# Kernel tuning notes

Measured on AMD Instinct MI355X. Metric: run time of the kernel, lower is better.

The kernel has to match this reference:

```python
import jax, jax.numpy as jnp
import numpy as np


def setup_inputs() -> dict:
    key = jax.random.key(0)
    k1, k2 = jax.random.split(key)
    b, d = 8192, 256
    x = jax.random.normal(k1, (b, d), dtype=jnp.float32)
    dc = jax.random.uniform(k2, (b, d), dtype=jnp.float32)
    dc_param = jnp.array([0.05], dtype=jnp.float32)
    return {"x": x, "dc": dc, "dc_param": dc_param}


def reference(x, dc, dc_param):
    # Faithful to torch: sim[i,j] = 1 / mean_k[(1-p)*(x[i,k]-x[j,k])^2
    #                                        + p*exp(1-dc[i,k])*exp(1-dc[j,k])]
    # Expanded to GEMMs to avoid the O(b^2*d) broadcast intermediate:
    #   mean_k (x_i - x_j)^2 = (|x_i|^2 + |x_j|^2 - 2 x_i.x_j) / d
    #   mean_k e_i[k] e_j[k] = (e_i . e_j) / d,  e = exp(1 - dc)
    b, d = x.shape
    p = dc_param[0]
    sq = jnp.sum(x * x, axis=1)                      # (b,)
    msd = (sq[:, None] + sq[None, :] - 2.0 * (x @ x.T)) / d  # (b,b)
    e = jnp.exp(1.0 - dc)                            # (b,d)
    mker = (e @ e.T) / d                             # (b,b)
    sim = 1.0 / ((1.0 - p) * msd + p * mker)
    eye = jnp.eye(b, dtype=x.dtype)
    return sim * (1.0 - eye) + eye
```

## Files before the change

### kernel.cpp

```cpp
#include <hip/hip_runtime.h>
#include <hip/hip_bf16.h>

typedef __attribute__((ext_vector_type(8))) __bf16 bf16x8;
typedef __attribute__((ext_vector_type(4))) float  f32x4;

constexpr int NROW = 8192;
constexpr int DDIM = 256;
constexpr int KDIM = 512;
constexpr int BM = 128, BN = 128, BK = 32;

__device__ __forceinline__ void gload_lds16(const void* g, void* l) {
  __builtin_amdgcn_global_load_lds(
      (const __attribute__((address_space(1))) void*)g,
      (__attribute__((address_space(3))) void*)l, 16, 0, 0);
}

__global__ __launch_bounds__(256) void prep_kernel(
    const float* __restrict__ x, const float* __restrict__ dc,
    const float* __restrict__ pparm,
    __hip_bfloat16* __restrict__ P, float* __restrict__ s)
{
  const int row = blockIdx.x;
  const int t   = threadIdx.x;
  const float xv = x[(size_t)row * DDIM + t];
  const float ev = __expf(1.0f - dc[(size_t)row * DDIM + t]);
  P[(size_t)row * KDIM + t]        = __float2bfloat16(xv);
  P[(size_t)row * KDIM + DDIM + t] = __float2bfloat16(ev);

  float v = xv * xv;
  #pragma unroll
  for (int off = 32; off > 0; off >>= 1) v += __shfl_down(v, off, 64);
  __shared__ float red[4];
  const int lane = t & 63, wid = t >> 6;
  if (lane == 0) red[wid] = v;
  __syncthreads();
  if (t == 0) {
    const float p = pparm[0];
    s[row] = (1.0f - p) * (1.0f / (float)DDIM) * (red[0] + red[1] + red[2] + red[3]);
  }
}

__global__ __launch_bounds__(256) void adj_gemm(
    const __hip_bfloat16* __restrict__ P, const float* __restrict__ s,
    const float* __restrict__ pparm, float* __restrict__ out)
{
  __shared__ __align__(16) __hip_bfloat16 As[BM * BK];
  __shared__ __align__(16) __hip_bfloat16 Bs[BN * BK];

  const float p  = pparm[0];
  const float cx = -2.0f * (1.0f - p) / (float)DDIM;
  const float ce = p / (float)DDIM;
  const float midscale = cx / ce;

  const int orig  = blockIdx.x;
  const int xcd   = orig & 7;
  const int local = orig >> 3;
  const int bi = xcd * 8 + (local & 7);
  const int bj = local >> 3;
  const int rowBase = bi * BM;
  const int colBase = bj * BN;

  const int t    = threadIdx.x;
  const int lane = t & 63;
  const int wid  = t >> 6;
  const int wr   = wid >> 1, wc = wid & 1;

  f32x4 acc[4][4];
  #pragma unroll
  for (int m = 0; m < 4; ++m)
    #pragma unroll
    for (int n = 0; n < 4; ++n)
      acc[m][n] = (f32x4){0.f, 0.f, 0.f, 0.f};

  const int frow = lane & 15;
  const int kq   = lane >> 4;

  const int q0 = wid * 64 + lane;
  const int q1 = q0 + 256;

  for (int kt = 0; kt < KDIM / BK; ++kt) {
    const int k0 = kt * BK;
    __syncthreads();
    {
      const __hip_bfloat16* ga0 = P + (size_t)(rowBase + (q0 >> 2)) * KDIM + k0 + (q0 & 3) * 8;
      gload_lds16(ga0, As + wid * 512);
      const __hip_bfloat16* ga1 = P + (size_t)(rowBase + (q1 >> 2)) * KDIM + k0 + (q1 & 3) * 8;
      gload_lds16(ga1, As + 2048 + wid * 512);
      const __hip_bfloat16* gb0 = P + (size_t)(colBase + (q0 >> 2)) * KDIM + k0 + (q0 & 3) * 8;
      gload_lds16(gb0, Bs + wid * 512);
      const __hip_bfloat16* gb1 = P + (size_t)(colBase + (q1 >> 2)) * KDIM + k0 + (q1 & 3) * 8;
      gload_lds16(gb1, Bs + 2048 + wid * 512);
    }
    __syncthreads();

    bf16x8 a[4], b[4];
    #pragma unroll
    for (int m = 0; m < 4; ++m)
      a[m] = *(const bf16x8*)(As + (wr * 64 + m * 16 + frow) * BK + kq * 8);
    #pragma unroll
    for (int n = 0; n < 4; ++n)
      b[n] = *(const bf16x8*)(Bs + (wc * 64 + n * 16 + frow) * BK + kq * 8);

    #pragma unroll
    for (int m = 0; m < 4; ++m)
      #pragma unroll
      for (int n = 0; n < 4; ++n)
        acc[m][n] = __builtin_amdgcn_mfma_f32_16x16x32_bf16(a[m], b[n], acc[m][n], 0, 0, 0);

    if (kt == (DDIM / BK) - 1) {
      #pragma unroll
      for (int m = 0; m < 4; ++m)
        #pragma unroll
        for (int n = 0; n < 4; ++n)
          acc[m][n] *= midscale;
    }
  }

  #pragma unroll
  for (int m = 0; m < 4; ++m) {
    const int growb = rowBase + wr * 64 + m * 16 + (lane >> 4) * 4;
    float srow[4];
    #pragma unroll
    for (int r = 0; r < 4; ++r) srow[r] = s[growb + r];
    #pragma unroll
    for (int n = 0; n < 4; ++n) {
      const int gcol = colBase + wc * 64 + n * 16 + (lane & 15);
      const float scol = s[gcol];
      #pragma unroll
      for (int r = 0; r < 4; ++r) {
        const int grow = growb + r;
        const float denom = srow[r] + scol + ce * acc[m][n][r];
        const float val = (grow == gcol) ? 1.0f : __builtin_amdgcn_rcpf(denom);
        out[(size_t)grow * NROW + gcol] = val;
      }
    }
  }
}

extern "C" void kernel_launch(void* const* d_in, const int* in_sizes, int n_in,
                              void* d_out, int out_size, void* d_ws, size_t ws_size,
                              hipStream_t stream) {
  const float* x  = (const float*)d_in[0];
  const float* dc = (const float*)d_in[1];
  const float* pp = (const float*)d_in[2];
  float* out = (float*)d_out;

  __hip_bfloat16* P = (__hip_bfloat16*)d_ws;
  float* s = (float*)((char*)d_ws + (size_t)NROW * KDIM * 2);

  prep_kernel<<<NROW, 256, 0, stream>>>(x, dc, pp, P, s);
  adj_gemm<<<(NROW / BM) * (NROW / BN), 256, 0, stream>>>(P, s, pp, out);
}
```

Baseline: 111.8 us.

## Triple-buffer LDS pipeline with larger 256x128x64 tiles and swizzled layout

Replaces the single-buffered 128x128x32 GEMM loop with a 256x128x64 tile, 512 threads, and a three-deep LDS ring filled by direct global-to-LDS loads issued two iterations ahead. Waits use explicit vmcnt counts and raw barriers instead of a pair of __syncthreads per step. LDS reads use an XOR swizzle to reduce bank conflicts, and MFMA sections are bracketed with s_setprio. The aim is to hide global load latency behind MFMA work and to get more reuse per tile. The cost is more LDS per block, hand-tuned wait counts that must match the load pattern exactly, and a changed block-to-XCD mapping.

New measurement: 106.4 us. 4.8% less time.

```diff
diff --git a/kernel.cpp b/kernel.cpp
--- a/kernel.cpp
+++ b/kernel.cpp
@@ -7,7 +7,13 @@
 constexpr int NROW = 8192;
 constexpr int DDIM = 256;
 constexpr int KDIM = 512;
-constexpr int BM = 128, BN = 128, BK = 32;
+constexpr int BM = 256, BN = 128, BK = 64;
+constexpr int NT = KDIM / BK;
+constexpr int ABYTES = BM * BK * 2;
+constexpr int BBYTES = BN * BK * 2;
+constexpr int BUFBYTES = ABYTES + BBYTES;
+constexpr int NBUF = 3;
+constexpr int LDS_TOTAL = NBUF * BUFBYTES;
 
 __device__ __forceinline__ void gload_lds16(const void* g, void* l) {
   __builtin_amdgcn_global_load_lds(
@@ -40,12 +46,11 @@
   }
 }
 
-__global__ __launch_bounds__(256) void adj_gemm(
+__global__ void __launch_bounds__(512, 2) adj_gemm(
     const __hip_bfloat16* __restrict__ P, const float* __restrict__ s,
     const float* __restrict__ pparm, float* __restrict__ out)
 {
-  __shared__ __align__(16) __hip_bfloat16 As[BM * BK];
-  __shared__ __align__(16) __hip_bfloat16 Bs[BN * BK];
+  extern __shared__ char lds[];
 
   const float p  = pparm[0];
   const float cx = -2.0f * (1.0f - p) / (float)DDIM;
@@ -53,17 +58,45 @@
   const float midscale = cx / ce;
 
   const int orig  = blockIdx.x;
-  const int xcd   = orig & 7;
+  const int x     = orig & 7;
   const int local = orig >> 3;
-  const int bi = xcd * 8 + (local & 7);
-  const int bj = local >> 3;
+  const int bi = x * 4 + (local & 3);
+  const int bj = local >> 2;
   const int rowBase = bi * BM;
   const int colBase = bj * BN;
 
-  const int t    = threadIdx.x;
-  const int lane = t & 63;
-  const int wid  = t >> 6;
-  const int wr   = wid >> 1, wc = wid & 1;
+  const int tid  = threadIdx.x;
+  const int lane = tid & 63;
+  const int wid  = tid >> 6;
+  const int wrow = (wid >> 1) * 64;
+  const int wcol = (wid & 1) * 64;
+  const int frow = lane & 15;
+  const int kq   = lane >> 4;
+
+  const char* Pc = (const char*)P;
+  const char* gsrc[6];
+  int ldst[6];
+  #pragma unroll
+  for (int j = 0; j < 4; ++j) {
+    const int o  = (j * 512 + tid) * 16;
+    const int r  = o >> 7;
+    const int cb = (o & 127) ^ (((o >> 9) & 1) << 5);
+    gsrc[j] = Pc + ((size_t)(rowBase + r) * KDIM) * 2 + cb;
+    ldst[j] = o;
+  }
+  #pragma unroll
+  for (int j = 0; j < 2; ++j) {
+    const int o  = (j * 512 + tid) * 16;
+    const int r  = o >> 7;
+    const int cb = (o & 127) ^ (((o >> 9) & 1) << 5);
+    gsrc[4 + j] = Pc + ((size_t)(colBase + r) * KDIM) * 2 + cb;
+    ldst[4 + j] = ABYTES + o;
+  }
+
+  #pragma unroll
+  for (int j = 0; j < 6; ++j) gload_lds16(gsrc[j],       lds + ldst[j]);
+  #pragma unroll
+  for (int j = 0; j < 6; ++j) gload_lds16(gsrc[j] + 128, lds + BUFBYTES + ldst[j]);
 
   f32x4 acc[4][4];
   #pragma unroll
@@ -72,42 +105,73 @@
     for (int n = 0; n < 4; ++n)
       acc[m][n] = (f32x4){0.f, 0.f, 0.f, 0.f};
 
-  const int frow = lane & 15;
-  const int kq   = lane >> 4;
-
-  const int q0 = wid * 64 + lane;
-  const int q1 = q0 + 256;
-
-  for (int kt = 0; kt < KDIM / BK; ++kt) {
-    const int k0 = kt * BK;
-    __syncthreads();
-    {
-      const __hip_bfloat16* ga0 = P + (size_t)(rowBase + (q0 >> 2)) * KDIM + k0 + (q0 & 3) * 8;
-      gload_lds16(ga0, As + wid * 512);
-      const __hip_bfloat16* ga1 = P + (size_t)(rowBase + (q1 >> 2)) * KDIM + k0 + (q1 & 3) * 8;
-      gload_lds16(ga1, As + 2048 + wid * 512);
-      const __hip_bfloat16* gb0 = P + (size_t)(colBase + (q0 >> 2)) * KDIM + k0 + (q0 & 3) * 8;
-      gload_lds16(gb0, Bs + wid * 512);
-      const __hip_bfloat16* gb1 = P + (size_t)(colBase + (q1 >> 2)) * KDIM + k0 + (q1 & 3) * 8;
-      gload_lds16(gb1, Bs + 2048 + wid * 512);
-    }
-    __syncthreads();
-
-    bf16x8 a[4], b[4];
+  #pragma unroll
+  for (int t = 0; t < NT; ++t) {
+    if (t < NT - 1) asm volatile("s_waitcnt vmcnt(6)" ::: "memory");
+    else            asm volatile("s_waitcnt vmcnt(0)" ::: "memory");
+    asm volatile("s_barrier" ::: "memory");
+
+    char* buf  = lds + (t % NBUF) * BUFBYTES;
+    char* nbuf = lds + ((t + 2) % NBUF) * BUFBYTES;
+    const int gadv = (t + 2) * (BK * 2);
+
+    bf16x8 a[4][2], bb[4][2];
     #pragma unroll
     for (int m = 0; m < 4; ++m)
-      a[m] = *(const bf16x8*)(As + (wr * 64 + m * 16 + frow) * BK + kq * 8);
-    #pragma unroll
-    for (int n = 0; n < 4; ++n)
-      b[n] = *(const bf16x8*)(Bs + (wc * 64 + n * 16 + frow) * BK + kq * 8);
-
+      #pragma unroll
+      for (int ks = 0; ks < 2; ++ks) {
+        const int row = wrow + m * 16 + frow;
+        const int cb  = (ks * 64 + kq * 16) ^ (((row >> 2) & 1) << 5);
+        a[m][ks] = *(const bf16x8*)(buf + row * 128 + cb);
+      }
+    #pragma unroll
+    for (int n = 0; n < 2; ++n)
+      #pragma unroll
+      for (int ks = 0; ks < 2; ++ks) {
+        const int row = wcol + n * 16 + frow;
+        const int cb  = (ks * 64 + kq * 16) ^ (((row >> 2) & 1) << 5);
+        bb[n][ks] = *(const bf16x8*)(buf + ABYTES + row * 128 + cb);
+      }
+    if (t + 2 < NT) {
+      gload_lds16(gsrc[0] + gadv, nbuf + ldst[0]);
+      gload_lds16(gsrc[1] + gadv, nbuf + ldst[1]);
+      gload_lds16(gsrc[2] + gadv, nbuf + ldst[2]);
+    }
+    __builtin_amdgcn_s_setprio(1);
     #pragma unroll
     for (int m = 0; m < 4; ++m)
       #pragma unroll
-      for (int n = 0; n < 4; ++n)
-        acc[m][n] = __builtin_amdgcn_mfma_f32_16x16x32_bf16(a[m], b[n], acc[m][n], 0, 0, 0);
-
-    if (kt == (DDIM / BK) - 1) {
+      for (int n = 0; n < 2; ++n)
+        #pragma unroll
+        for (int ks = 0; ks < 2; ++ks)
+          acc[m][n] = __builtin_amdgcn_mfma_f32_16x16x32_bf16(a[m][ks], bb[n][ks], acc[m][n], 0, 0, 0);
+    __builtin_amdgcn_s_setprio(0);
+    asm volatile("s_barrier" ::: "memory");
+
+    #pragma unroll
+    for (int n = 2; n < 4; ++n)
+      #pragma unroll
+      for (int ks = 0; ks < 2; ++ks) {
+        const int row = wcol + n * 16 + frow;
+        const int cb  = (ks * 64 + kq * 16) ^ (((row >> 2) & 1) << 5);
+        bb[n][ks] = *(const bf16x8*)(buf + ABYTES + row * 128 + cb);
+      }
+    if (t + 2 < NT) {
+      gload_lds16(gsrc[3] + gadv, nbuf + ldst[3]);
+      gload_lds16(gsrc[4] + gadv, nbuf + ldst[4]);
+      gload_lds16(gsrc[5] + gadv, nbuf + ldst[5]);
+    }
+    __builtin_amdgcn_s_setprio(1);
+    #pragma unroll
+    for (int m = 0; m < 4; ++m)
+      #pragma unroll
+      for (int n = 2; n < 4; ++n)
+        #pragma unroll
+        for (int ks = 0; ks < 2; ++ks)
+          acc[m][n] = __builtin_amdgcn_mfma_f32_16x16x32_bf16(a[m][ks], bb[n][ks], acc[m][n], 0, 0, 0);
+    __builtin_amdgcn_s_setprio(0);
+
+    if (t == DDIM / BK - 1) {
       #pragma unroll
       for (int m = 0; m < 4; ++m)
         #pragma unroll
@@ -118,13 +182,13 @@
 
   #pragma unroll
   for (int m = 0; m < 4; ++m) {
-    const int growb = rowBase + wr * 64 + m * 16 + (lane >> 4) * 4;
+    const int growb = rowBase + wrow + m * 16 + (lane >> 4) * 4;
     float srow[4];
     #pragma unroll
     for (int r = 0; r < 4; ++r) srow[r] = s[growb + r];
     #pragma unroll
     for (int n = 0; n < 4; ++n) {
-      const int gcol = colBase + wc * 64 + n * 16 + (lane & 15);
+      const int gcol = colBase + wcol + n * 16 + (lane & 15);
       const float scol = s[gcol];
       #pragma unroll
       for (int r = 0; r < 4; ++r) {
@@ -148,6 +212,9 @@
   __hip_bfloat16* P = (__hip_bfloat16*)d_ws;
   float* s = (float*)((char*)d_ws + (size_t)NROW * KDIM * 2);
 
+  hipFuncSetAttribute(reinterpret_cast<const void*>(adj_gemm),
+                      hipFuncAttributeMaxDynamicSharedMemorySize, LDS_TOTAL);
+
   prep_kernel<<<NROW, 256, 0, stream>>>(x, dc, pp, P, s);
-  adj_gemm<<<(NROW / BM) * (NROW / BN), 256, 0, stream>>>(P, s, pp, out);
-}
+  adj_gemm<<<(NROW / BM) * (NROW / BN), 512, LDS_TOTAL, stream>>>(P, s, pp, out);
+}
```

## Double-buffer LDS tiles with swizzle and enlarge GEMM block to 256x128

Applied to the files above, without the earlier changes.

Switches the GEMM to a 256x128 tile handled by 512 threads (8 waves) with double-buffered LDS, so the global-to-LDS load for the next K-step is issued before computing on the current one. It drops one barrier per K-step and applies an XOR swizzle to the LDS layout to cut bank conflicts on fragment reads. The XCD-aware block mapping is adjusted for the new grid. The kernel is output-write bound (256 MB fp32 output), so the gains may be limited, and the larger block raises LDS and register use per CU.

Result: slower. 115.3 us (+3.1%).

```diff
diff --git a/kernel.cpp b/kernel.cpp
--- a/kernel.cpp
+++ b/kernel.cpp
@@ -7,7 +7,11 @@
 constexpr int NROW = 8192;
 constexpr int DDIM = 256;
 constexpr int KDIM = 512;
-constexpr int BM = 128, BN = 128, BK = 32;
+constexpr int BM = 256, BN = 128, BK = 32;
+constexpr int NT = KDIM / BK;
+constexpr int ABYTES = BM * BK * 2;
+constexpr int BBYTES = BN * BK * 2;
+constexpr int BUFBYTES = ABYTES + BBYTES;
 
 __device__ __forceinline__ void gload_lds16(const void* g, void* l) {
   __builtin_amdgcn_global_load_lds(
@@ -40,12 +44,11 @@
   }
 }
 
-__global__ __launch_bounds__(256) void adj_gemm(
+__global__ void __launch_bounds__(512, 4) adj_gemm(
     const __hip_bfloat16* __restrict__ P, const float* __restrict__ s,
     const float* __restrict__ pparm, float* __restrict__ out)
 {
-  __shared__ __align__(16) __hip_bfloat16 As[BM * BK];
-  __shared__ __align__(16) __hip_bfloat16 Bs[BN * BK];
+  __shared__ __align__(16) char lds[2 * BUFBYTES];
 
   const float p  = pparm[0];
   const float cx = -2.0f * (1.0f - p) / (float)DDIM;
@@ -55,15 +58,40 @@
   const int orig  = blockIdx.x;
   const int xcd   = orig & 7;
   const int local = orig >> 3;
-  const int bi = xcd * 8 + (local & 7);
-  const int bj = local >> 3;
+  const int bi = xcd * 4 + (local & 3);
+  const int bj = local >> 2;
   const int rowBase = bi * BM;
   const int colBase = bj * BN;
 
-  const int t    = threadIdx.x;
-  const int lane = t & 63;
-  const int wid  = t >> 6;
-  const int wr   = wid >> 1, wc = wid & 1;
+  const int tid  = threadIdx.x;
+  const int lane = tid & 63;
+  const int wid  = tid >> 6;
+  const int wmrow = (wid >> 1) * 64;
+  const int wnrow = (wid & 1) * 64;
+  const int frow = lane & 15;
+  const int kq   = lane >> 4;
+
+  const int cb = (kq * 16) ^ ((frow & 3) << 4);
+
+  const int rA0  = tid >> 2;
+  const int gcol = ((tid & 3) * 16) ^ ((rA0 & 3) << 4);
+  const char* Pc = (const char*)P;
+  const char* gA0 = Pc + (size_t)(rowBase + rA0)       * (KDIM * 2) + gcol;
+  const char* gA1 = Pc + (size_t)(rowBase + 128 + rA0) * (KDIM * 2) + gcol;
+  const char* gB  = Pc + (size_t)(colBase + rA0)       * (KDIM * 2) + gcol;
+  const int dA0 = tid * 16, dA1 = 8192 + tid * 16, dB = ABYTES + tid * 16;
+
+#define STAGE(kk) do {                                   \
+    char* _b = lds + ((kk) & 1) * BUFBYTES;              \
+    const int _ko = (kk) * (BK * 2);                     \
+    gload_lds16(gA0 + _ko, _b + dA0);                    \
+    gload_lds16(gA1 + _ko, _b + dA1);                    \
+    gload_lds16(gB  + _ko, _b + dB);                     \
+  } while (0)
+
+  STAGE(0);
+  asm volatile("s_waitcnt vmcnt(0)" ::: "memory");
+  asm volatile("s_barrier" ::: "memory");
 
   f32x4 acc[4][4];
   #pragma unroll
@@ -72,66 +100,55 @@
     for (int n = 0; n < 4; ++n)
       acc[m][n] = (f32x4){0.f, 0.f, 0.f, 0.f};
 
-  const int frow = lane & 15;
-  const int kq   = lane >> 4;
+  #pragma unroll
+  for (int t = 0; t < NT; ++t) {
+    const char* buf  = lds + (t & 1) * BUFBYTES;
+    const char* bufB = buf + ABYTES;
 
-  const int q0 = wid * 64 + lane;
-  const int q1 = q0 + 256;
-
-  for (int kt = 0; kt < KDIM / BK; ++kt) {
-    const int k0 = kt * BK;
-    __syncthreads();
-    {
-      const __hip_bfloat16* ga0 = P + (size_t)(rowBase + (q0 >> 2)) * KDIM + k0 + (q0 & 3) * 8;
-      gload_lds16(ga0, As + wid * 512);
-      const __hip_bfloat16* ga1 = P + (size_t)(rowBase + (q1 >> 2)) * KDIM + k0 + (q1 & 3) * 8;
-      gload_lds16(ga1, As + 2048 + wid * 512);
-      const __hip_bfloat16* gb0 = P + (size_t)(colBase + (q0 >> 2)) * KDIM + k0 + (q0 & 3) * 8;
-      gload_lds16(gb0, Bs + wid * 512);
-      const __hip_bfloat16* gb1 = P + (size_t)(colBase + (q1 >> 2)) * KDIM + k0 + (q1 & 3) * 8;
-      gload_lds16(gb1, Bs + 2048 + wid * 512);
-    }
-    __syncthreads();
+    if (t < NT - 1) STAGE(t + 1);
 
     bf16x8 a[4], b[4];
     #pragma unroll
-    for (int m = 0; m < 4; ++m)
-      a[m] = *(const bf16x8*)(As + (wr * 64 + m * 16 + frow) * BK + kq * 8);
+    for (int i = 0; i < 4; ++i)
+      a[i] = *(const bf16x8*)(buf + (wmrow + i * 16 + frow) * 64 + cb);
     #pragma unroll
-    for (int n = 0; n < 4; ++n)
-      b[n] = *(const bf16x8*)(Bs + (wc * 64 + n * 16 + frow) * BK + kq * 8);
+    for (int j = 0; j < 4; ++j)
+      b[j] = *(const bf16x8*)(bufB + (wnrow + j * 16 + frow) * 64 + cb);
 
     #pragma unroll
-    for (int m = 0; m < 4; ++m)
+    for (int i = 0; i < 4; ++i)
       #pragma unroll
-      for (int n = 0; n < 4; ++n)
-        acc[m][n] = __builtin_amdgcn_mfma_f32_16x16x32_bf16(a[m], b[n], acc[m][n], 0, 0, 0);
+      for (int j = 0; j < 4; ++j)
+        acc[i][j] = __builtin_amdgcn_mfma_f32_16x16x32_bf16(a[i], b[j], acc[i][j], 0, 0, 0);
 
-    if (kt == (DDIM / BK) - 1) {
+    if (t == DDIM / BK - 1) {
       #pragma unroll
       for (int m = 0; m < 4; ++m)
         #pragma unroll
         for (int n = 0; n < 4; ++n)
           acc[m][n] *= midscale;
     }
+
+    if (t < NT - 1) {
+      asm volatile("s_waitcnt vmcnt(0)" ::: "memory");
+      asm volatile("s_barrier" ::: "memory");
+    }
   }
 
+  const int rq = lane >> 4;
   #pragma unroll
-  for (int m = 0; m < 4; ++m) {
-    const int growb = rowBase + wr * 64 + m * 16 + (lane >> 4) * 4;
-    float srow[4];
+  for (int n = 0; n < 4; ++n) {
+    const int gcol_o = colBase + wnrow + n * 16 + frow;
+    const float scol = s[gcol_o];
     #pragma unroll
-    for (int r = 0; r < 4; ++r) srow[r] = s[growb + r];
-    #pragma unroll
-    for (int n = 0; n < 4; ++n) {
-      const int gcol = colBase + wc * 64 + n * 16 + (lane & 15);
-      const float scol = s[gcol];
+    for (int m = 0; m < 4; ++m) {
+      const int growb = rowBase + wmrow + m * 16 + rq * 4;
       #pragma unroll
       for (int r = 0; r < 4; ++r) {
         const int grow = growb + r;
-        const float denom = srow[r] + scol + ce * acc[m][n][r];
-        const float val = (grow == gcol) ? 1.0f : __builtin_amdgcn_rcpf(denom);
-        out[(size_t)grow * NROW + gcol] = val;
+        const float denom = s[grow] + scol + ce * acc[m][n][r];
+        const float val = (grow == gcol_o) ? 1.0f : __builtin_amdgcn_rcpf(denom);
+        out[(size_t)grow * NROW + gcol_o] = val;
       }
     }
   }
@@ -149,5 +166,5 @@
   float* s = (float*)((char*)d_ws + (size_t)NROW * KDIM * 2);
 
   prep_kernel<<<NROW, 256, 0, stream>>>(x, dc, pp, P, s);
-  adj_gemm<<<(NROW / BM) * (NROW / BN), 256, 0, stream>>>(P, s, pp, out);
+  adj_gemm<<<(NROW / BM) * (NROW / BN), 512, 0, stream>>>(P, s, pp, out);
 }
```
